# Kernel tuning notes

Measured on AMD Instinct MI355X. Metric: run time of the kernel, lower is better.

## Reference

```python
import jax, jax.numpy as jnp
import numpy as np

D_MODEL, N_HEAD, D_FFN = 1024, 16, 4096
MAX_REL = 128
NUM_BUCKETS = 2 * MAX_REL - 1  # 255
B, T = 2, 2048


def algebraic_ln(x, gamma, beta, a, b_raw, eps=1e-5):
    mean = jnp.mean(x, axis=-1, keepdims=True)
    var = jnp.var(x, axis=-1, keepdims=True)  # unbiased=False
    z = var + eps
    b = jax.nn.softplus(10.0 * b_raw) / 10.0  # softplus with beta=10
    p = a[0] + a[1] * z + a[2] * z ** 2
    q = b[0] + b[1] * z + b[2] * z ** 2
    return (x - mean) * (p / q) * gamma + beta


def setup_inputs() -> dict:
    key = jax.random.key(0)
    ks = jax.random.split(key, 16)
    s = (1.0 / np.sqrt(D_MODEL)).astype(np.float32)
    inp = {
        'x': jax.random.normal(ks[0], (B, T, D_MODEL), jnp.float32),
        'casual_mask': jnp.tril(jnp.ones((T, T), dtype=bool)),
        'Wq': jax.random.normal(ks[1], (D_MODEL, D_MODEL), jnp.float32) * s,
        'bq': jnp.zeros((D_MODEL,), jnp.float32),
        'Wk': jax.random.normal(ks[2], (D_MODEL, D_MODEL), jnp.float32) * s,
        'bk': jnp.zeros((D_MODEL,), jnp.float32),
        'Wv': jax.random.normal(ks[3], (D_MODEL, D_MODEL), jnp.float32) * s,
        'bv': jnp.zeros((D_MODEL,), jnp.float32),
        'Wo': jax.random.normal(ks[4], (D_MODEL, D_MODEL), jnp.float32) * s,
        'bo': jnp.zeros((D_MODEL,), jnp.float32),
        'rel_emb': jax.random.normal(ks[5], (NUM_BUCKETS, N_HEAD), jnp.float32) * 0.02,
        'g1': jnp.ones((D_MODEL,), jnp.float32),
        'be1': jnp.zeros((D_MODEL,), jnp.float32),
        'a1': jnp.array([1.0, 0.5, 0.1], jnp.float32),
        'br1': jnp.array([1.0, 0.3, 0.05], jnp.float32),
        'g2': jnp.ones((D_MODEL,), jnp.float32),
        'be2': jnp.zeros((D_MODEL,), jnp.float32),
        'a2': jnp.array([1.0, 0.5, 0.1], jnp.float32),
        'br2': jnp.array([1.0, 0.3, 0.05], jnp.float32),
        'W1': jax.random.normal(ks[6], (D_FFN, D_MODEL), jnp.float32) * s,
        'b1': jnp.zeros((D_FFN,), jnp.float32),
        'W2': jax.random.normal(ks[7], (D_MODEL, D_FFN), jnp.float32) * (1.0 / np.sqrt(D_FFN)),
        'b2': jnp.zeros((D_MODEL,), jnp.float32),
        'res_scale': jnp.array(0.5, jnp.float32),
    }
    return inp


def attention(x, mask, Wq, bq, Wk, bk, Wv, bv, Wo, bo, rel_emb):
    Bx, Tx, C = x.shape
    H, Dh = N_HEAD, C // N_HEAD
    scale = Dh ** -0.5
    Q = (x @ Wq.T + bq).reshape(Bx, Tx, H, Dh)
    K = (x @ Wk.T + bk).reshape(Bx, Tx, H, Dh)
    V = (x @ Wv.T + bv).reshape(Bx, Tx, H, Dh)
    scores = jnp.einsum('bqhd,bkhd->bhqk', Q, K) * scale
    rel = jnp.arange(Tx)[None, :] - jnp.arange(Tx)[:, None]  # k_pos - q_pos
    buckets = jnp.clip(rel, -MAX_REL + 1, MAX_REL - 1) + (MAX_REL - 1)
    bias = rel_emb[buckets]  # [T,T,H]
    scores = scores + jnp.transpose(bias, (2, 0, 1))[None]
    m = mask[None, None]  # [1,1,T,T]
    # torch: masked_fill(-inf) then masked_fill(0) -> masked entries become 0
    scores = jnp.where(m, scores, 0.0)
    w = jax.nn.relu(scores) + 1e-6
    w = jnp.where(m, w, 0.0)
    w = w / (jnp.sum(w, axis=-1, keepdims=True) + 1e-6)
    out = jnp.einsum('bhqk,bkhd->bqhd', w, V).reshape(Bx, Tx, C)
    return out @ Wo.T + bo


def reference(x, casual_mask, Wq, bq, Wk, bk, Wv, bv, Wo, bo, rel_emb,
              g1, be1, a1, br1, g2, be2, a2, br2, W1, b1, W2, b2, res_scale):
    scale = jnp.clip(res_scale, 0.2, 1.0)
    x = x + scale * attention(algebraic_ln(x, g1, be1, a1, br1), casual_mask,
                              Wq, bq, Wk, bk, Wv, bv, Wo, bo, rel_emb)
    h = algebraic_ln(x, g2, be2, a2, br2)
    ffn = jax.nn.relu(h @ W1.T + b1) @ W2.T + b2  # dropout is identity at eval
    return x + scale * ffn
```

## Files before the change

### kernel.cpp

```cpp
#include <hip/hip_runtime.h>
#include <stdint.h>


#define D_MODEL 1024
#define T_SEQ   2048
#define NHEAD   16
#define DH      64
#define DFFN    4096
#define MROWS   4096

using short8  = __attribute__((ext_vector_type(8))) short;
using floatx4 = __attribute__((ext_vector_type(4))) float;

__device__ __forceinline__ float bf2f(ushort u) {
    union { uint32_t i; float f; } x; x.i = ((uint32_t)u) << 16; return x.f;
}
__device__ __forceinline__ ushort f2bf(float f) {
    union { float f; uint32_t i; } x; x.f = f;
    uint32_t i = x.i;
    return (ushort)((i + 0x7fffu + ((i >> 16) & 1u)) >> 16);
}
__device__ __forceinline__ float ldf(const void* p, size_t i, int dt) {
    return dt ? bf2f(((const ushort*)p)[i]) : ((const float*)p)[i];
}
__device__ __forceinline__ int detect_bf16(const void* g1) {
    return *(const uint32_t*)g1 == 0x3F803F80u;
}
__device__ __forceinline__ void gld_lds16(const void* g, void* l) {
    __builtin_amdgcn_global_load_lds(
        (__attribute__((address_space(1))) uint32_t*)(g),
        (__attribute__((address_space(3))) uint32_t*)(l), 16, 0, 0);
}
__device__ __forceinline__ float softplus10(float t) {
    float u = 10.f * t;
    return (u > 20.f ? u : log1pf(expf(u))) * 0.1f;
}

template <int INMODE>
__global__ __launch_bounds__(256)
void ln_kernel(const void* __restrict__ xin,
               const void* __restrict__ gamma, const void* __restrict__ beta,
               const void* __restrict__ a3, const void* __restrict__ br3,
               ushort* __restrict__ out, const void* __restrict__ dtprobe)
{
    const int dt = detect_bf16(dtprobe);
    const int row = blockIdx.x;
    const int tid = threadIdx.x;
    const int col = tid * 4;
    float v[4];
    if (INMODE == 1) {
        const float* x = (const float*)xin + (size_t)row * D_MODEL;
        float4 t = *(const float4*)(x + col);
        v[0] = t.x; v[1] = t.y; v[2] = t.z; v[3] = t.w;
    } else if (dt) {
        const ushort* x = (const ushort*)xin + (size_t)row * D_MODEL;
        ushort4 t = *(const ushort4*)(x + col);
        v[0] = bf2f(t.x); v[1] = bf2f(t.y); v[2] = bf2f(t.z); v[3] = bf2f(t.w);
    } else {
        const float* x = (const float*)xin + (size_t)row * D_MODEL;
        float4 t = *(const float4*)(x + col);
        v[0] = t.x; v[1] = t.y; v[2] = t.z; v[3] = t.w;
    }
    float s  = v[0] + v[1] + v[2] + v[3];
    float s2 = v[0]*v[0] + v[1]*v[1] + v[2]*v[2] + v[3]*v[3];
#pragma unroll
    for (int m = 32; m > 0; m >>= 1) {
        s  += __shfl_down(s,  m, 64);
        s2 += __shfl_down(s2, m, 64);
    }
    __shared__ float wsum[4], wsum2[4];
    const int wave = tid >> 6, lane = tid & 63;
    if (lane == 0) { wsum[wave] = s; wsum2[wave] = s2; }
    __syncthreads();
    s  = wsum[0] + wsum[1] + wsum[2] + wsum[3];
    s2 = wsum2[0] + wsum2[1] + wsum2[2] + wsum2[3];
    const float mean = s * (1.f / D_MODEL);
    const float var  = s2 * (1.f / D_MODEL) - mean * mean;
    const float z = var + 1e-5f;
    const float a0 = ldf(a3, 0, dt), a1 = ldf(a3, 1, dt), a2 = ldf(a3, 2, dt);
    const float b0 = softplus10(ldf(br3, 0, dt));
    const float b1 = softplus10(ldf(br3, 1, dt));
    const float b2 = softplus10(ldf(br3, 2, dt));
    const float p = a0 + a1 * z + a2 * z * z;
    const float q = b0 + b1 * z + b2 * z * z;
    const float f = p / q;
    ushort4 o; ushort* op = (ushort*)&o;
#pragma unroll
    for (int e = 0; e < 4; e++) {
        op[e] = f2bf((v[e] - mean) * f * ldf(gamma, col + e, dt) + ldf(beta, col + e, dt));
    }
    *(ushort4*)(out + (size_t)row * D_MODEL + col) = o;
}

template <int MODE, int BM, int BN>
__global__ __launch_bounds__(256)
void gemm_bt(const ushort* __restrict__ A,
             const void* __restrict__ Bw0, const void* __restrict__ Bw1,
             const void* __restrict__ Bw2,
             const void* __restrict__ bias0, const void* __restrict__ bias1,
             const void* __restrict__ bias2,
             void* __restrict__ C0, void* __restrict__ C1, void* __restrict__ C2v,
             const void* __restrict__ resid, const void* __restrict__ scale_p,
             int Nst, int K, const void* __restrict__ dtprobe)
{
    constexpr int NI = BM / 32;
    constexpr int NJ = BN / 32;
    constexpr int AC = BM / 64;
    constexpr int BC = BN / 64;
    __shared__ __align__(16) ushort As[BM * 32];
    __shared__ __align__(16) ushort Bs[BN * 32];
    const int dt = detect_bf16(dtprobe);
    const int tid  = threadIdx.x;
    const int wave = tid >> 6, lane = tid & 63;
    const int wr = wave >> 1, wc = wave & 1;
    const int g = lane >> 4, l15 = lane & 15;

    const void* Bw = Bw0; const void* bias = bias0; void* Cout = C0;
    if (MODE == 4) {
        const int mat = blockIdx.x >> 3;
        if (mat == 1)      { Bw = Bw1; bias = bias1; Cout = C1; }
        else if (mat == 2) { Bw = Bw2; bias = bias2; Cout = C2v; }
    }
    const int m0 = blockIdx.y * BM;
    const int n0 = (MODE == 4) ? ((blockIdx.x & 7) * 128) : (blockIdx.x * BN);

    floatx4 acc[NI][NJ];
#pragma unroll
    for (int i = 0; i < NI; i++)
#pragma unroll
        for (int j = 0; j < NJ; j++) acc[i][j] = {0.f, 0.f, 0.f, 0.f};

    const int srow = lane >> 2;
    const int ssw  = (srow >> 1) & 3;
    const int scol = (((lane & 3) ^ ssw) * 8);
    const int fsw  = (l15 >> 1) & 3;
    for (int k0 = 0; k0 < K; k0 += 32) {
        __syncthreads();
        if (dt) {
            const ushort* Bb = (const ushort*)Bw;
#pragma unroll
            for (int c = 0; c < AC; c++) {
                const int r0 = (wave * AC + c) * 16;
                gld_lds16(A + (size_t)(m0 + r0 + srow) * K + k0 + scol, &As[r0 * 32]);
            }
#pragma unroll
            for (int c = 0; c < BC; c++) {
                const int r0 = (wave * BC + c) * 16;
                gld_lds16(Bb + (size_t)(n0 + r0 + srow) * K + k0 + scol, &Bs[r0 * 32]);
            }
        } else {
            const float* Bf = (const float*)Bw;
#pragma unroll
            for (int c = 0; c < AC; c++) {
                const int r0 = (wave * AC + c) * 16;
                gld_lds16(A + (size_t)(m0 + r0 + srow) * K + k0 + scol, &As[r0 * 32]);
            }
#pragma unroll
            for (int c = 0; c < BC; c++) {
                const int r0 = (wave * BC + c) * 16;
                const float* src = Bf + (size_t)(n0 + r0 + srow) * K + k0 + scol;
                float4 t0 = *(const float4*)(src);
                float4 t1 = *(const float4*)(src + 4);
                ushort tmp[8] = { f2bf(t0.x), f2bf(t0.y), f2bf(t0.z), f2bf(t0.w),
                                  f2bf(t1.x), f2bf(t1.y), f2bf(t1.z), f2bf(t1.w) };
                *(short8*)&Bs[(r0 + srow) * 32 + (lane & 3) * 8] = *(short8*)tmp;
            }
        }
        __syncthreads();
        short8 af[NI], bfr[NJ];
#pragma unroll
        for (int i = 0; i < NI; i++)
            af[i]  = *(const short8*)&As[(wr * (BM / 2) + i * 16 + l15) * 32 + ((g ^ fsw) * 8)];
#pragma unroll
        for (int j = 0; j < NJ; j++)
            bfr[j] = *(const short8*)&Bs[(wc * (BN / 2) + j * 16 + l15) * 32 + ((g ^ fsw) * 8)];
#pragma unroll
        for (int i = 0; i < NI; i++)
#pragma unroll
            for (int j = 0; j < NJ; j++)
                acc[i][j] = __builtin_amdgcn_mfma_f32_16x16x32_bf16(af[i], bfr[j], acc[i][j], 0, 0, 0);
    }

    float scl = 0.f;
    if (MODE == 2 || MODE == 3) scl = fminf(fmaxf(ldf(scale_p, 0, dt), 0.2f), 1.0f);
#pragma unroll
    for (int i = 0; i < NI; i++) {
        const int rowb = m0 + wr * (BM / 2) + i * 16 + g * 4;
#pragma unroll
        for (int j = 0; j < NJ; j++) {
            const int col = n0 + wc * (BN / 2) + j * 16 + l15;
            const float bi = ldf(bias, col, dt);
#pragma unroll
            for (int r = 0; r < 4; r++) {
                const size_t idx = (size_t)(rowb + r) * Nst + col;
                const float v = acc[i][j][r] + bi;
                if (MODE == 0 || MODE == 4) ((ushort*)Cout)[idx] = f2bf(v);
                else if (MODE == 1) ((ushort*)Cout)[idx] = f2bf(fmaxf(v, 0.f));
                else if (MODE == 2) ((float*)Cout)[idx]  = ldf(resid, idx, dt) + scl * v;
                else {
                    const float o = ((const float*)resid)[idx] + scl * v;
                    if (dt) ((ushort*)Cout)[idx] = f2bf(o);
                    else    ((float*)Cout)[idx]  = o;
                }
            }
        }
    }
}

__global__ __launch_bounds__(256)
void attn_kernel(const ushort* __restrict__ Q, const ushort* __restrict__ K,
                 const ushort* __restrict__ V, const void* __restrict__ rel,
                 ushort* __restrict__ Out, const void* __restrict__ dtprobe)
{
    __shared__ __align__(16) ushort Qs[128 * 64];
    __shared__ __align__(16) ushort Ks[64 * 64];
    __shared__ __align__(16) ushort Vt[64 * 88];
    __shared__ __align__(16) ushort Ss[128 * 88];
    __shared__ float rel_h[128];
    __shared__ float den_lds[128];

    const int dt = detect_bf16(dtprobe);
    const int tid  = threadIdx.x;
    const int wave = tid >> 6, lane = tid & 63;
    const int wr = wave >> 1, wc = wave & 1;
    const int g = lane >> 4, l15 = lane & 15;
    const int qi = blockIdx.x, h = blockIdx.y, b = blockIdx.z;

    if (tid < 128) {
        rel_h[tid] = ldf(rel, (size_t)tid * NHEAD + h, dt);
        den_lds[tid] = 0.f;
    }

    const ushort* Qg = Q + ((size_t)(b * T_SEQ + qi * 128)) * D_MODEL + h * DH;
    {
        const int lrow = lane >> 3, pch = lane & 7;
#pragma unroll
        for (int c = 0; c < 4; c++) {
            const int r0 = (wave * 4 + c) * 8;
            const int row = r0 + lrow;
            gld_lds16(Qg + (size_t)row * D_MODEL + ((pch ^ (row & 7)) * 8), &Qs[r0 * 64]);
        }
    }

    floatx4 onum[4][2];
#pragma unroll
    for (int i = 0; i < 4; i++) { onum[i][0] = {0.f,0.f,0.f,0.f}; onum[i][1] = {0.f,0.f,0.f,0.f}; }
    float den_p[4][4];
#pragma unroll
    for (int i = 0; i < 4; i++)
#pragma unroll
        for (int r = 0; r < 4; r++) den_p[i][r] = 0.f;

    const int nk = 2 * (qi + 1);
    const float scale = 0.125f;

    for (int kt = 0; kt < nk; kt++) {
        const int kbase = kt * 64;
        __syncthreads();
        const ushort* Kg = K + ((size_t)(b * T_SEQ + kbase)) * D_MODEL + h * DH;
        {
            const int lrow = lane >> 3, pch = lane & 7;
#pragma unroll
            for (int c = 0; c < 2; c++) {
                const int r0 = (wave * 2 + c) * 8;
                const int row = r0 + lrow;
                gld_lds16(Kg + (size_t)row * D_MODEL + ((pch ^ (row & 7)) * 8), &Ks[r0 * 64]);
            }
        }
        const ushort* Vg = V + ((size_t)(b * T_SEQ + kbase)) * D_MODEL + h * DH;
#pragma unroll
        for (int c = 0; c < 2; c++) {
            const int chunk = tid + c * 256;
            const int krow = chunk >> 3;
            const int dcol = (chunk & 7) * 8;
            short8 t = *(const short8*)(Vg + (size_t)krow * D_MODEL + dcol);
            ushort tmp[8]; *(short8*)tmp = t;
#pragma unroll
            for (int e = 0; e < 8; e++) Vt[(dcol + e) * 88 + krow] = tmp[e];
        }
        __syncthreads();

        floatx4 sacc[4][2];
#pragma unroll
        for (int i = 0; i < 4; i++) { sacc[i][0] = {0.f,0.f,0.f,0.f}; sacc[i][1] = {0.f,0.f,0.f,0.f}; }
#pragma unroll
        for (int ks = 0; ks < 2; ks++) {
            short8 qa[4], kb[2];
            const int ch = ks * 4 + g;
#pragma unroll
            for (int i = 0; i < 4; i++) {
                const int row = wr * 64 + i * 16 + l15;
                qa[i] = *(const short8*)&Qs[row * 64 + ((ch ^ (row & 7)) * 8)];
            }
#pragma unroll
            for (int j = 0; j < 2; j++) {
                const int row = wc * 32 + j * 16 + l15;
                kb[j] = *(const short8*)&Ks[row * 64 + ((ch ^ (row & 7)) * 8)];
            }
#pragma unroll
            for (int i = 0; i < 4; i++)
#pragma unroll
                for (int j = 0; j < 2; j++)
                    sacc[i][j] = __builtin_amdgcn_mfma_f32_16x16x32_bf16(qa[i], kb[j], sacc[i][j], 0, 0, 0);
        }
#pragma unroll
        for (int i = 0; i < 4; i++) {
            const int qrow = wr * 64 + i * 16 + g * 4;
#pragma unroll
            for (int j = 0; j < 2; j++) {
                const int kcol = wc * 32 + j * 16 + l15;
                const int kg = kbase + kcol;
#pragma unroll
                for (int r = 0; r < 4; r++) {
                    const int qg = qi * 128 + qrow + r;
                    const int d = qg - kg;
                    float w = 0.f;
                    if (d >= 0) {
                        const int bucket = 127 - (d < 127 ? d : 127);
                        const float sv = sacc[i][j][r] * scale + rel_h[bucket];
                        w = fmaxf(sv, 0.f) + 1e-6f;
                    }
                    den_p[i][r] += w;
                    Ss[(qrow + r) * 88 + kcol] = f2bf(w);
                }
            }
        }
        __syncthreads();

#pragma unroll
        for (int ks = 0; ks < 2; ks++) {
            short8 wa[4], vb[2];
#pragma unroll
            for (int i = 0; i < 4; i++)
                wa[i] = *(const short8*)&Ss[(wr * 64 + i * 16 + l15) * 88 + ks * 32 + g * 8];
#pragma unroll
            for (int j = 0; j < 2; j++)
                vb[j] = *(const short8*)&Vt[(wc * 32 + j * 16 + l15) * 88 + ks * 32 + g * 8];
#pragma unroll
            for (int i = 0; i < 4; i++)
#pragma unroll
                for (int j = 0; j < 2; j++)
                    onum[i][j] = __builtin_amdgcn_mfma_f32_16x16x32_bf16(wa[i], vb[j], onum[i][j], 0, 0, 0);
        }
    }

#pragma unroll
    for (int i = 0; i < 4; i++)
#pragma unroll
        for (int r = 0; r < 4; r++) {
            float v = den_p[i][r];
            v += __shfl_xor(v, 1, 64);
            v += __shfl_xor(v, 2, 64);
            v += __shfl_xor(v, 4, 64);
            v += __shfl_xor(v, 8, 64);
            den_p[i][r] = v;
        }
    __syncthreads();
    if (l15 == 0) {
#pragma unroll
        for (int i = 0; i < 4; i++)
#pragma unroll
            for (int r = 0; r < 4; r++)
                atomicAdd(&den_lds[wr * 64 + i * 16 + g * 4 + r], den_p[i][r]);
    }
    __syncthreads();

    const size_t obase = ((size_t)(b * T_SEQ + qi * 128)) * D_MODEL + h * DH;
#pragma unroll
    for (int i = 0; i < 4; i++) {
        const int qrow = wr * 64 + i * 16 + g * 4;
#pragma unroll
        for (int j = 0; j < 2; j++) {
            const int dcol = wc * 32 + j * 16 + l15;
#pragma unroll
            for (int r = 0; r < 4; r++) {
                const float dn = den_lds[qrow + r] + 1e-6f;
                Out[obase + (size_t)(qrow + r) * D_MODEL + dcol] = f2bf(onum[i][j][r] / dn);
            }
        }
    }
}

extern "C" void kernel_launch(void* const* d_in, const int* in_sizes, int n_in,
                              void* d_out, int out_size, void* d_ws, size_t ws_size,
                              hipStream_t stream)
{
    const void* x   = d_in[0];
    const void* Wq  = d_in[2];
    const void* bq  = d_in[3];
    const void* Wk  = d_in[4];
    const void* bk  = d_in[5];
    const void* Wv  = d_in[6];
    const void* bv  = d_in[7];
    const void* Wo  = d_in[8];
    const void* bo  = d_in[9];
    const void* rel = d_in[10];
    const void* g1  = d_in[11];
    const void* be1 = d_in[12];
    const void* a1  = d_in[13];
    const void* br1 = d_in[14];
    const void* g2  = d_in[15];
    const void* be2 = d_in[16];
    const void* a2  = d_in[17];
    const void* br2 = d_in[18];
    const void* W1  = d_in[19];
    const void* b1  = d_in[20];
    const void* W2  = d_in[21];
    const void* b2  = d_in[22];
    const void* rs  = d_in[23];

    char* ws = (char*)d_ws;
    ushort* ln1  = (ushort*)(ws);
    ushort* Qb   = (ushort*)(ws + (8u  << 20));
    ushort* Kb   = (ushort*)(ws + (16u << 20));
    ushort* Vb   = (ushort*)(ws + (24u << 20));
    ushort* atb  = (ushort*)(ws + (32u << 20));
    float*  x1   = (float*)(ws + (40u << 20));
    ushort* hbuf = (ushort*)(ws + (56u << 20));
    ushort* ffn1 = (ushort*)(ws);

    const dim3 blk(256);

    ln_kernel<0><<<dim3(MROWS), blk, 0, stream>>>(x, g1, be1, a1, br1, ln1, g1);
    gemm_bt<4, 128, 128><<<dim3(24, MROWS / 128), blk, 0, stream>>>(
        ln1, Wq, Wk, Wv, bq, bk, bv, Qb, Kb, Vb,
        nullptr, nullptr, D_MODEL, D_MODEL, g1);
    attn_kernel<<<dim3(T_SEQ / 128, NHEAD, 2), blk, 0, stream>>>(Qb, Kb, Vb, rel, atb, g1);
    gemm_bt<2, 64, 64><<<dim3(D_MODEL / 64, MROWS / 64), blk, 0, stream>>>(
        atb, Wo, nullptr, nullptr, bo, nullptr, nullptr, x1, nullptr, nullptr,
        x, rs, D_MODEL, D_MODEL, g1);
    ln_kernel<1><<<dim3(MROWS), blk, 0, stream>>>(x1, g2, be2, a2, br2, hbuf, g1);
    gemm_bt<1, 128, 128><<<dim3(DFFN / 128, MROWS / 128), blk, 0, stream>>>(
        hbuf, W1, nullptr, nullptr, b1, nullptr, nullptr, ffn1, nullptr, nullptr,
        nullptr, nullptr, DFFN, D_MODEL, g1);
    gemm_bt<3, 64, 64><<<dim3(D_MODEL / 64, MROWS / 64), blk, 0, stream>>>(
        ffn1, W2, nullptr, nullptr, b2, nullptr, nullptr, d_out, nullptr, nullptr,
        x1, rs, D_MODEL, DFFN, g1);
}
```

Before: 570.0 us.

## Pair causal query tiles per block and shrink attention tile to 64 rows

New measurement: 516.3 us. -9.4%, faster.

```diff
diff --git a/kernel.cpp b/kernel.cpp
--- a/kernel.cpp
+++ b/kernel.cpp
@@ -212,170 +212,187 @@
                  const ushort* __restrict__ V, const void* __restrict__ rel,
                  ushort* __restrict__ Out, const void* __restrict__ dtprobe)
 {
-    __shared__ __align__(16) ushort Qs[128 * 64];
     __shared__ __align__(16) ushort Ks[64 * 64];
     __shared__ __align__(16) ushort Vt[64 * 88];
-    __shared__ __align__(16) ushort Ss[128 * 88];
+    __shared__ __align__(16) ushort Ss[64 * 88];
     __shared__ float rel_h[128];
-    __shared__ float den_lds[128];
+    __shared__ float den_l[64];
 
     const int dt = detect_bf16(dtprobe);
     const int tid  = threadIdx.x;
     const int wave = tid >> 6, lane = tid & 63;
     const int wr = wave >> 1, wc = wave & 1;
     const int g = lane >> 4, l15 = lane & 15;
-    const int qi = blockIdx.x, h = blockIdx.y, b = blockIdx.z;
-
-    if (tid < 128) {
-        rel_h[tid] = ldf(rel, (size_t)tid * NHEAD + h, dt);
-        den_lds[tid] = 0.f;
-    }
-
-    const ushort* Qg = Q + ((size_t)(b * T_SEQ + qi * 128)) * D_MODEL + h * DH;
-    {
-        const int lrow = lane >> 3, pch = lane & 7;
-#pragma unroll
-        for (int c = 0; c < 4; c++) {
-            const int r0 = (wave * 4 + c) * 8;
-            const int row = r0 + lrow;
-            gld_lds16(Qg + (size_t)row * D_MODEL + ((pch ^ (row & 7)) * 8), &Qs[r0 * 64]);
+    const int pair = blockIdx.x, h = blockIdx.y, b = blockIdx.z;
+
+    if (tid < 128) rel_h[tid] = ldf(rel, (size_t)tid * NHEAD + h, dt);
+    const float scale = 0.125f;
+
+    for (int ph = 0; ph < 2; ph++) {
+        const int qt = ph ? (31 - pair) : pair;
+        __syncthreads();
+        if (tid < 64) den_l[tid] = 0.f;
+
+        const ushort* Qg = Q + ((size_t)(b * T_SEQ + qt * 64)) * D_MODEL + h * DH;
+        short8 qa[2][2];
+#pragma unroll
+        for (int i = 0; i < 2; i++)
+#pragma unroll
+            for (int ks = 0; ks < 2; ks++)
+                qa[i][ks] = *(const short8*)(Qg + (size_t)(wr * 32 + i * 16 + l15) * D_MODEL
+                                             + (ks * 4 + g) * 8);
+
+        floatx4 onum[2][2];
+#pragma unroll
+        for (int i = 0; i < 2; i++) { onum[i][0] = {0.f,0.f,0.f,0.f}; onum[i][1] = {0.f,0.f,0.f,0.f}; }
+        float den_p[2][4];
+#pragma unroll
+        for (int i = 0; i < 2; i++)
+#pragma unroll
+            for (int r = 0; r < 4; r++) den_p[i][r] = 0.f;
+
+        const int nk = qt + 1;
+        for (int kt = 0; kt < nk; kt++) {
+            const int kbase = kt * 64;
+            __syncthreads();
+            const ushort* Kg = K + ((size_t)(b * T_SEQ + kbase)) * D_MODEL + h * DH;
+            {
+                const int lrow = lane >> 3, pch = lane & 7;
+#pragma unroll
+                for (int c = 0; c < 2; c++) {
+                    const int r0 = (wave * 2 + c) * 8;
+                    const int row = r0 + lrow;
+                    gld_lds16(Kg + (size_t)row * D_MODEL + ((pch ^ (row & 7)) * 8), &Ks[r0 * 64]);
+                }
+            }
+            const ushort* Vg = V + ((size_t)(b * T_SEQ + kbase)) * D_MODEL + h * DH;
+#pragma unroll
+            for (int c = 0; c < 2; c++) {
+                const int chunk = tid + c * 256;
+                const int krow = chunk >> 3;
+                const int bb   = chunk & 7;
+                short8 t = *(const short8*)(Vg + (size_t)krow * D_MODEL + bb * 8);
+                ushort tmp[8]; *(short8*)tmp = t;
+#pragma unroll
+                for (int e = 0; e < 8; e++) {
+                    const int ee = (e + bb) & 7;
+                    Vt[(bb * 8 + ee) * 88 + krow] = tmp[ee];
+                }
+            }
+            __syncthreads();
+
+            floatx4 sacc[2][2];
+#pragma unroll
+            for (int i = 0; i < 2; i++) { sacc[i][0] = {0.f,0.f,0.f,0.f}; sacc[i][1] = {0.f,0.f,0.f,0.f}; }
+#pragma unroll
+            for (int ks = 0; ks < 2; ks++) {
+                short8 kb[2];
+                const int ch = ks * 4 + g;
+#pragma unroll
+                for (int j = 0; j < 2; j++) {
+                    const int row = wc * 32 + j * 16 + l15;
+                    kb[j] = *(const short8*)&Ks[row * 64 + ((ch ^ (row & 7)) * 8)];
+                }
+#pragma unroll
+                for (int i = 0; i < 2; i++)
+#pragma unroll
+                    for (int j = 0; j < 2; j++)
+                        sacc[i][j] = __builtin_amdgcn_mfma_f32_16x16x32_bf16(qa[i][ks], kb[j], sacc[i][j], 0, 0, 0);
+            }
+
+            const int dq = qt - kt;
+            if (dq >= 3) {
+                const float c0 = rel_h[0];
+#pragma unroll
+                for (int i = 0; i < 2; i++) {
+                    const int qrow = wr * 32 + i * 16 + g * 4;
+#pragma unroll
+                    for (int j = 0; j < 2; j++) {
+                        const int kcol = wc * 32 + j * 16 + l15;
+#pragma unroll
+                        for (int r = 0; r < 4; r++) {
+                            const float w = fmaxf(sacc[i][j][r] * scale + c0, 0.f) + 1e-6f;
+                            den_p[i][r] += w;
+                            Ss[(qrow + r) * 88 + kcol] = f2bf(w);
+                        }
+                    }
+                }
+            } else {
+#pragma unroll
+                for (int i = 0; i < 2; i++) {
+                    const int qrow = wr * 32 + i * 16 + g * 4;
+#pragma unroll
+                    for (int j = 0; j < 2; j++) {
+                        const int kcol = wc * 32 + j * 16 + l15;
+                        const int kg = kbase + kcol;
+#pragma unroll
+                        for (int r = 0; r < 4; r++) {
+                            const int qg = qt * 64 + qrow + r;
+                            const int d = qg - kg;
+                            float w = 0.f;
+                            if (d >= 0) {
+                                const int bucket = 127 - (d < 127 ? d : 127);
+                                const float sv = sacc[i][j][r] * scale + rel_h[bucket];
+                                w = fmaxf(sv, 0.f) + 1e-6f;
+                            }
+                            den_p[i][r] += w;
+                            Ss[(qrow + r) * 88 + kcol] = f2bf(w);
+                        }
+                    }
+                }
+            }
+            __syncthreads();
+
+#pragma unroll
+            for (int ks = 0; ks < 2; ks++) {
+                short8 wa[2], vb[2];
+#pragma unroll
+                for (int i = 0; i < 2; i++)
+                    wa[i] = *(const short8*)&Ss[(wr * 32 + i * 16 + l15) * 88 + ks * 32 + g * 8];
+#pragma unroll
+                for (int j = 0; j < 2; j++)
+                    vb[j] = *(const short8*)&Vt[(wc * 32 + j * 16 + l15) * 88 + ks * 32 + g * 8];
+#pragma unroll
+                for (int i = 0; i < 2; i++)
+#pragma unroll
+                    for (int j = 0; j < 2; j++)
+                        onum[i][j] = __builtin_amdgcn_mfma_f32_16x16x32_bf16(wa[i], vb[j], onum[i][j], 0, 0, 0);
+            }
         }
-    }
-
-    floatx4 onum[4][2];
-#pragma unroll
-    for (int i = 0; i < 4; i++) { onum[i][0] = {0.f,0.f,0.f,0.f}; onum[i][1] = {0.f,0.f,0.f,0.f}; }
-    float den_p[4][4];
-#pragma unroll
-    for (int i = 0; i < 4; i++)
-#pragma unroll
-        for (int r = 0; r < 4; r++) den_p[i][r] = 0.f;
-
-    const int nk = 2 * (qi + 1);
-    const float scale = 0.125f;
-
-    for (int kt = 0; kt < nk; kt++) {
-        const int kbase = kt * 64;
+
+#pragma unroll
+        for (int i = 0; i < 2; i++)
+#pragma unroll
+            for (int r = 0; r < 4; r++) {
+                float v = den_p[i][r];
+                v += __shfl_xor(v, 1, 64);
+                v += __shfl_xor(v, 2, 64);
+                v += __shfl_xor(v, 4, 64);
+                v += __shfl_xor(v, 8, 64);
+                den_p[i][r] = v;
+            }
         __syncthreads();
-        const ushort* Kg = K + ((size_t)(b * T_SEQ + kbase)) * D_MODEL + h * DH;
-        {
-            const int lrow = lane >> 3, pch = lane & 7;
-#pragma unroll
-            for (int c = 0; c < 2; c++) {
-                const int r0 = (wave * 2 + c) * 8;
-                const int row = r0 + lrow;
-                gld_lds16(Kg + (size_t)row * D_MODEL + ((pch ^ (row & 7)) * 8), &Ks[r0 * 64]);
-            }
-        }
-        const ushort* Vg = V + ((size_t)(b * T_SEQ + kbase)) * D_MODEL + h * DH;
-#pragma unroll
-        for (int c = 0; c < 2; c++) {
-            const int chunk = tid + c * 256;
-            const int krow = chunk >> 3;
-            const int dcol = (chunk & 7) * 8;
-            short8 t = *(const short8*)(Vg + (size_t)krow * D_MODEL + dcol);
-            ushort tmp[8]; *(short8*)tmp = t;
-#pragma unroll
-            for (int e = 0; e < 8; e++) Vt[(dcol + e) * 88 + krow] = tmp[e];
+        if (l15 == 0) {
+#pragma unroll
+            for (int i = 0; i < 2; i++)
+#pragma unroll
+                for (int r = 0; r < 4; r++)
+                    atomicAdd(&den_l[wr * 32 + i * 16 + g * 4 + r], den_p[i][r]);
         }
         __syncthreads();
 
-        floatx4 sacc[4][2];
-#pragma unroll
-        for (int i = 0; i < 4; i++) { sacc[i][0] = {0.f,0.f,0.f,0.f}; sacc[i][1] = {0.f,0.f,0.f,0.f}; }
-#pragma unroll
-        for (int ks = 0; ks < 2; ks++) {
-            short8 qa[4], kb[2];
-            const int ch = ks * 4 + g;
-#pragma unroll
-            for (int i = 0; i < 4; i++) {
-                const int row = wr * 64 + i * 16 + l15;
-                qa[i] = *(const short8*)&Qs[row * 64 + ((ch ^ (row & 7)) * 8)];
-            }
+        const size_t obase = ((size_t)(b * T_SEQ + qt * 64)) * D_MODEL + h * DH;
+#pragma unroll
+        for (int i = 0; i < 2; i++) {
+            const int qrow = wr * 32 + i * 16 + g * 4;
 #pragma unroll
             for (int j = 0; j < 2; j++) {
-                const int row = wc * 32 + j * 16 + l15;
-                kb[j] = *(const short8*)&Ks[row * 64 + ((ch ^ (row & 7)) * 8)];
-            }
-#pragma unroll
-            for (int i = 0; i < 4; i++)
-#pragma unroll
-                for (int j = 0; j < 2; j++)
-                    sacc[i][j] = __builtin_amdgcn_mfma_f32_16x16x32_bf16(qa[i], kb[j], sacc[i][j], 0, 0, 0);
-        }
-#pragma unroll
-        for (int i = 0; i < 4; i++) {
-            const int qrow = wr * 64 + i * 16 + g * 4;
-#pragma unroll
-            for (int j = 0; j < 2; j++) {
-                const int kcol = wc * 32 + j * 16 + l15;
-                const int kg = kbase + kcol;
+                const int dcol = wc * 32 + j * 16 + l15;
 #pragma unroll
                 for (int r = 0; r < 4; r++) {
-                    const int qg = qi * 128 + qrow + r;
-                    const int d = qg - kg;
-                    float w = 0.f;
-                    if (d >= 0) {
-                        const int bucket = 127 - (d < 127 ? d : 127);
-                        const float sv = sacc[i][j][r] * scale + rel_h[bucket];
-                        w = fmaxf(sv, 0.f) + 1e-6f;
-                    }
-                    den_p[i][r] += w;
-                    Ss[(qrow + r) * 88 + kcol] = f2bf(w);
-                }
-            }
-        }
-        __syncthreads();
-
-#pragma unroll
-        for (int ks = 0; ks < 2; ks++) {
-            short8 wa[4], vb[2];
-#pragma unroll
-            for (int i = 0; i < 4; i++)
-                wa[i] = *(const short8*)&Ss[(wr * 64 + i * 16 + l15) * 88 + ks * 32 + g * 8];
-#pragma unroll
-            for (int j = 0; j < 2; j++)
-                vb[j] = *(const short8*)&Vt[(wc * 32 + j * 16 + l15) * 88 + ks * 32 + g * 8];
-#pragma unroll
-            for (int i = 0; i < 4; i++)
-#pragma unroll
-                for (int j = 0; j < 2; j++)
-                    onum[i][j] = __builtin_amdgcn_mfma_f32_16x16x32_bf16(wa[i], vb[j], onum[i][j], 0, 0, 0);
-        }
-    }
-
-#pragma unroll
-    for (int i = 0; i < 4; i++)
-#pragma unroll
-        for (int r = 0; r < 4; r++) {
-            float v = den_p[i][r];
-            v += __shfl_xor(v, 1, 64);
-            v += __shfl_xor(v, 2, 64);
-            v += __shfl_xor(v, 4, 64);
-            v += __shfl_xor(v, 8, 64);
-            den_p[i][r] = v;
-        }
-    __syncthreads();
-    if (l15 == 0) {
-#pragma unroll
-        for (int i = 0; i < 4; i++)
-#pragma unroll
-            for (int r = 0; r < 4; r++)
-                atomicAdd(&den_lds[wr * 64 + i * 16 + g * 4 + r], den_p[i][r]);
-    }
-    __syncthreads();
-
-    const size_t obase = ((size_t)(b * T_SEQ + qi * 128)) * D_MODEL + h * DH;
-#pragma unroll
-    for (int i = 0; i < 4; i++) {
-        const int qrow = wr * 64 + i * 16 + g * 4;
-#pragma unroll
-        for (int j = 0; j < 2; j++) {
-            const int dcol = wc * 32 + j * 16 + l15;
-#pragma unroll
-            for (int r = 0; r < 4; r++) {
-                const float dn = den_lds[qrow + r] + 1e-6f;
-                Out[obase + (size_t)(qrow + r) * D_MODEL + dcol] = f2bf(onum[i][j][r] / dn);
+                    const float dn = den_l[qrow + r] + 1e-6f;
+                    Out[obase + (size_t)(qrow + r) * D_MODEL + dcol] = f2bf(onum[i][j][r] / dn);
+                }
             }
         }
     }
@@ -425,7 +442,7 @@
     gemm_bt<4, 128, 128><<<dim3(24, MROWS / 128), blk, 0, stream>>>(
         ln1, Wq, Wk, Wv, bq, bk, bv, Qb, Kb, Vb,
         nullptr, nullptr, D_MODEL, D_MODEL, g1);
-    attn_kernel<<<dim3(T_SEQ / 128, NHEAD, 2), blk, 0, stream>>>(Qb, Kb, Vb, rel, atb, g1);
+    attn_kernel<<<dim3(16, NHEAD, 2), blk, 0, stream>>>(Qb, Kb, Vb, rel, atb, g1);
     gemm_bt<2, 64, 64><<<dim3(D_MODEL / 64, MROWS / 64), blk, 0, stream>>>(
         atb, Wo, nullptr, nullptr, bo, nullptr, nullptr, x1, nullptr, nullptr,
         x, rs, D_MODEL, D_MODEL, g1);
```
